# Kernel optimization log

Measured on AMD Instinct MI355X. Metric: run time of the kernel, lower is better.

## Reference

```python
import jax, jax.numpy as jnp
import numpy as np

G = 128          # voxel grid extent per axis
B = G + 2        # key base, allows coords in [-1, G] after +1 shift
N_PTS = 100000
C_IN = 32
C_OUT = 32


def _key(c):
    # c: [..., 3] int32 voxel coords in [-1, G]; unique linear key per voxel
    return ((c[..., 0] + 1) * B + (c[..., 1] + 1)) * B + (c[..., 2] + 1)


def setup_inputs() -> dict:
    key = jax.random.key(0)
    k1, k2, k3 = jax.random.split(key, 3)
    positions = jax.random.randint(k1, (N_PTS, 3), 0, G, dtype=jnp.int32)
    features = jax.random.normal(k2, (N_PTS, C_IN), dtype=jnp.float32)
    # per-offset filter matrices, [K^3, Cin, Cout], fan-in style init
    weight = jax.random.normal(k3, (27, C_IN, C_OUT), dtype=jnp.float32) * (1.0 / np.sqrt(27 * C_IN))
    return {"features": features, "positions": positions, "weight": weight}


def reference(features, positions, weight):
    # Submanifold sparse conv: output at the same sparse positions as input.
    # For each of the 27 kernel offsets, hash-lookup the neighbor voxel,
    # gather its feature (or 0 if absent), matmul with the per-offset filter,
    # accumulate. use_bias=False, normalize=False, voxel_size=1.0, offset=0.
    n = features.shape[0]
    keys = _key(positions)                      # [N]
    order = jnp.argsort(keys)
    sk = keys[order]                            # sorted keys (hash table)

    ax = jnp.arange(-1, 2, dtype=jnp.int32)
    off = jnp.stack(jnp.meshgrid(ax, ax, ax, indexing="ij"), axis=-1).reshape(27, 3)

    qk = _key(positions[None, :, :] + off[:, None, :])          # [27, N]
    pos_idx = jnp.clip(jnp.searchsorted(sk, qk), 0, n - 1)      # [27, N]
    match = sk[pos_idx] == qk                                   # neighbor exists?
    gidx = order[pos_idx]                                       # original index of neighbor

    gf = jnp.where(match[..., None], features[gidx], 0.0)       # [27, N, Cin] gather
    out = jnp.einsum("onc,ocd->nd", gf, weight)                 # scatter-accumulate via reduce over o
    return out
```

## Files before the change

kernel.cpp:

```cpp
#include <hip/hip_runtime.h>


#define GRID_B 130
#define GRID_CELLS 2197000
#define C 32
#define NTHR 256
#define PTS 64
#define CAP 24

__global__ void build_grid_kernel(const int* __restrict__ pos,
                                  int* __restrict__ grid, int n) {
    int i = blockIdx.x * blockDim.x + threadIdx.x;
    if (i >= n) return;
    int x = pos[3 * i + 0] + 1;
    int y = pos[3 * i + 1] + 1;
    int z = pos[3 * i + 2] + 1;
    atomicMax(&grid[(x * GRID_B + y) * GRID_B + z], n - i);
}

__global__ __launch_bounds__(NTHR)
void conv_kernel(const float* __restrict__ feat,
                 const int* __restrict__ pos,
                 const float* __restrict__ w,
                 const int* __restrict__ grid,
                 float* __restrict__ out, int n) {
    __shared__ int   s_cnt[27];
    __shared__ int   s_list[27][CAP];
    __shared__ int   s_rep[PTS];
    __shared__ float s_acc[PTS][C];

    const int tid = threadIdx.x;
    const int pt_base = blockIdx.x * PTS;

    if (tid < 27) s_cnt[tid] = 0;
    __syncthreads();

    for (int t = tid; t < PTS * 27; t += NTHR) {
        int pl = t / 27;
        int o  = t - pl * 27;
        int pt = pt_base + pl;
        if (pt < n) {
            int x = pos[3 * pt + 0] + (o / 9) - 1 + 1;
            int y = pos[3 * pt + 1] + ((o / 3) % 3) - 1 + 1;
            int z = pos[3 * pt + 2] + (o % 3) - 1 + 1;
            int v = grid[(x * GRID_B + y) * GRID_B + z];
            if (o == 13) {
                s_rep[pl] = n - v;
            } else if (v >= 1) {
                int slot = atomicAdd(&s_cnt[o], 1);
                if (slot < CAP) s_list[o][slot] = (pl << 17) | (n - v);
            }
        }
    }
    __syncthreads();

    {
        const int cout = tid & 31;
        float wreg[32];
        #pragma unroll
        for (int c = 0; c < 32; ++c) wreg[c] = w[13 * 1024 + c * 32 + cout];
        for (int u = tid; u < PTS * C; u += NTHR) {
            int pl = u >> 5;
            if (pt_base + pl < n) {
                const float4* __restrict__ f4 = (const float4*)(feat + (size_t)s_rep[pl] * C);
                float acc = 0.0f;
                #pragma unroll
                for (int k = 0; k < 8; ++k) {
                    float4 fv = f4[k];
                    acc = fmaf(fv.x, wreg[4 * k + 0], acc);
                    acc = fmaf(fv.y, wreg[4 * k + 1], acc);
                    acc = fmaf(fv.z, wreg[4 * k + 2], acc);
                    acc = fmaf(fv.w, wreg[4 * k + 3], acc);
                }
                s_acc[pl][cout] = acc;
            }
        }
    }
    __syncthreads();

    {
        const int wv = tid >> 6;
        const int lane = tid & 63;
        const int cout = lane & 31;
        const int half = lane >> 5;
        for (int o = wv; o < 27; o += 4) {
            if (o == 13) continue;
            int cnt = min(s_cnt[o], CAP);
            if (cnt == 0) continue;
            float wreg[32];
            #pragma unroll
            for (int c = 0; c < 32; ++c) wreg[c] = w[o * 1024 + c * 32 + cout];
            for (int e = half; e < cnt; e += 2) {
                int packed = s_list[o][e];
                int pl = packed >> 17;
                int j  = packed & 0x1FFFF;
                const float4* __restrict__ f4 = (const float4*)(feat + (size_t)j * C);
                float acc = 0.0f;
                #pragma unroll
                for (int k = 0; k < 8; ++k) {
                    float4 fv = f4[k];
                    acc = fmaf(fv.x, wreg[4 * k + 0], acc);
                    acc = fmaf(fv.y, wreg[4 * k + 1], acc);
                    acc = fmaf(fv.z, wreg[4 * k + 2], acc);
                    acc = fmaf(fv.w, wreg[4 * k + 3], acc);
                }
                atomicAdd(&s_acc[pl][cout], acc);
            }
        }
    }
    __syncthreads();

    {
        const int base = pt_base * C;
        const int lim = n * C - base;
        for (int u = tid; u < PTS * C && u < lim; u += NTHR)
            out[base + u] = s_acc[u >> 5][u & 31];
    }
}

extern "C" void kernel_launch(void* const* d_in, const int* in_sizes, int n_in,
                              void* d_out, int out_size, void* d_ws, size_t ws_size,
                              hipStream_t stream) {
    const float* features = (const float*)d_in[0];
    const int*   positions = (const int*)d_in[1];
    const float* weight = (const float*)d_in[2];
    float* out = (float*)d_out;
    const int n = in_sizes[0] / C;

    int* grid = (int*)d_ws;
    hipMemsetAsync(grid, 0, (size_t)GRID_CELLS * sizeof(int), stream);

    build_grid_kernel<<<(n + 255) / 256, 256, 0, stream>>>(positions, grid, n);

    conv_kernel<<<(n + PTS - 1) / PTS, NTHR, 0, stream>>>(features, positions, weight,
                                                          grid, out, n);
}
```

Before: 130.4 us.

## Add occupancy bitmap to probe z-neighbor triples with one load

Builds a one-bit-per-voxel occupancy bitmap next to the dense index grid. The neighbor search now reads two bitmap words per (dx,dy) column to find which of the three z-neighbors exist, and only touches the index grid for occupied cells. This replaces 27 scattered grid loads per point with 9 bitmap probes plus loads for the hits only. Positions are also staged in shared memory. It costs an extra atomicOr per point and a slightly larger memset.

```diff
diff --git a/kernel.cpp b/kernel.cpp
--- a/kernel.cpp
+++ b/kernel.cpp
@@ -3,19 +3,23 @@
 
 #define GRID_B 130
 #define GRID_CELLS 2197000
+#define BM_WORDS 68704
 #define C 32
 #define NTHR 256
 #define PTS 64
 #define CAP 24
 
 __global__ void build_grid_kernel(const int* __restrict__ pos,
-                                  int* __restrict__ grid, int n) {
+                                  int* __restrict__ grid,
+                                  unsigned int* __restrict__ bm, int n) {
     int i = blockIdx.x * blockDim.x + threadIdx.x;
     if (i >= n) return;
     int x = pos[3 * i + 0] + 1;
     int y = pos[3 * i + 1] + 1;
     int z = pos[3 * i + 2] + 1;
-    atomicMax(&grid[(x * GRID_B + y) * GRID_B + z], n - i);
+    int key = (x * GRID_B + y) * GRID_B + z;
+    atomicMax(&grid[key], n - i);
+    atomicOr(&bm[key >> 5], 1u << (key & 31));
 }
 
 __global__ __launch_bounds__(NTHR)
@@ -23,32 +27,48 @@
                  const int* __restrict__ pos,
                  const float* __restrict__ w,
                  const int* __restrict__ grid,
+                 const unsigned int* __restrict__ bm,
                  float* __restrict__ out, int n) {
     __shared__ int   s_cnt[27];
     __shared__ int   s_list[27][CAP];
     __shared__ int   s_rep[PTS];
+    __shared__ int   s_pos[PTS * 3];
     __shared__ float s_acc[PTS][C];
 
     const int tid = threadIdx.x;
     const int pt_base = blockIdx.x * PTS;
 
     if (tid < 27) s_cnt[tid] = 0;
+    for (int u = tid; u < PTS * 3; u += NTHR) {
+        int g = pt_base * 3 + u;
+        if (g < n * 3) s_pos[u] = pos[g];
+    }
     __syncthreads();
 
-    for (int t = tid; t < PTS * 27; t += NTHR) {
-        int pl = t / 27;
-        int o  = t - pl * 27;
-        int pt = pt_base + pl;
-        if (pt < n) {
-            int x = pos[3 * pt + 0] + (o / 9) - 1 + 1;
-            int y = pos[3 * pt + 1] + ((o / 3) % 3) - 1 + 1;
-            int z = pos[3 * pt + 2] + (o % 3) - 1 + 1;
-            int v = grid[(x * GRID_B + y) * GRID_B + z];
-            if (o == 13) {
-                s_rep[pl] = n - v;
-            } else if (v >= 1) {
-                int slot = atomicAdd(&s_cnt[o], 1);
-                if (slot < CAP) s_list[o][slot] = (pl << 17) | (n - v);
+    for (int t = tid; t < PTS * 9; t += NTHR) {
+        int pl = t / 9;
+        int xy = t - pl * 9;
+        if (pt_base + pl < n) {
+            int dx = xy / 3;
+            int dy = xy - dx * 3;
+            int x0 = s_pos[pl * 3 + 0] + dx;
+            int y0 = s_pos[pl * 3 + 1] + dy;
+            int k0 = (x0 * GRID_B + y0) * GRID_B + s_pos[pl * 3 + 2];
+            unsigned int w0 = bm[(k0 >> 5)];
+            unsigned int w1 = bm[(k0 >> 5) + 1];
+            unsigned int bits =
+                (unsigned int)((((unsigned long long)w1 << 32) | w0) >> (k0 & 31)) & 7u;
+            int obase = xy * 3;
+            if (xy == 4) {
+                s_rep[pl] = n - grid[k0 + 1];
+                bits &= 5u;
+            }
+            while (bits) {
+                int oz = __ffs(bits) - 1;
+                bits &= bits - 1;
+                int v = grid[k0 + oz];
+                int slot = atomicAdd(&s_cnt[obase + oz], 1);
+                if (slot < CAP) s_list[obase + oz][slot] = (pl << 17) | (n - v);
             }
         }
     }
@@ -128,10 +148,11 @@
     const int n = in_sizes[0] / C;
 
     int* grid = (int*)d_ws;
-    hipMemsetAsync(grid, 0, (size_t)GRID_CELLS * sizeof(int), stream);
+    unsigned int* bm = (unsigned int*)(grid + GRID_CELLS);
+    hipMemsetAsync(d_ws, 0, (size_t)(GRID_CELLS + BM_WORDS) * sizeof(int), stream);
 
-    build_grid_kernel<<<(n + 255) / 256, 256, 0, stream>>>(positions, grid, n);
+    build_grid_kernel<<<(n + 255) / 256, 256, 0, stream>>>(positions, grid, bm, n);
 
     conv_kernel<<<(n + PTS - 1) / PTS, NTHR, 0, stream>>>(features, positions, weight,
-                                                          grid, out, n);
+                                                          grid, bm, out, n);
 }
```

Measured after the change: 130.3 us. Within noise of the previous version (-0.1%).
